# Kernel tuning notes

Measured on AMD Instinct MI355X. Metric: run time of the kernel, lower is better.

The kernel has to match this reference:

```python
import jax, jax.numpy as jnp
import numpy as np

B, S, D = 4, 2048, 1024
H = 16
HD = D // H
FF = 4096
EPS = 1e-5

def _layernorm(x, g, b):
    mu = jnp.mean(x, axis=-1, keepdims=True)
    var = jnp.mean(jnp.square(x - mu), axis=-1, keepdims=True)
    return (x - mu) * jax.lax.rsqrt(var + EPS) * g + b

def setup_inputs() -> dict:
    key = jax.random.key(0)
    ks = jax.random.split(key, 12)
    s_attn = 1.0 / np.sqrt(D)
    s_ff1 = 1.0 / np.sqrt(D)
    s_ff2 = 1.0 / np.sqrt(FF)
    return {
        "x": jax.random.normal(ks[0], (B, S, D), jnp.float32),
        "ln1_g": jnp.ones((D,), jnp.float32),
        "ln1_b": jnp.zeros((D,), jnp.float32),
        "ln2_g": jnp.ones((D,), jnp.float32),
        "ln2_b": jnp.zeros((D,), jnp.float32),
        "Wq": jax.random.normal(ks[1], (D, D), jnp.float32) * s_attn,
        "Wk": jax.random.normal(ks[2], (D, D), jnp.float32) * s_attn,
        "Wv": jax.random.normal(ks[3], (D, D), jnp.float32) * s_attn,
        "Wo": jax.random.normal(ks[4], (D, D), jnp.float32) * s_attn,
        "W1": jax.random.normal(ks[5], (D, FF), jnp.float32) * s_ff1,
        "b1": jnp.zeros((FF,), jnp.float32),
        "W2": jax.random.normal(ks[6], (FF, D), jnp.float32) * s_ff2,
        "b2": jnp.zeros((D,), jnp.float32),
    }

def reference(x, ln1_g, ln1_b, ln2_g, ln2_b, Wq, Wk, Wv, Wo, W1, b1, W2, b2):
    # pre-LN self-attention (y = x), mask=None, dropout=0, attn proj bias=False
    h = _layernorm(x, ln1_g, ln1_b)                      # [B,S,D]
    q = (h @ Wq).reshape(B, S, H, HD).transpose(0, 2, 1, 3)  # [B,H,S,HD]
    k = (h @ Wk).reshape(B, S, H, HD).transpose(0, 2, 1, 3)
    v = (h @ Wv).reshape(B, S, H, HD).transpose(0, 2, 1, 3)
    scores = jnp.einsum('bhqd,bhkd->bhqk', q, k) / np.sqrt(HD)  # [B,H,S,S]
    attn = jax.nn.softmax(scores, axis=-1)
    o = jnp.einsum('bhqk,bhkd->bhqd', attn, v)           # [B,H,S,HD]
    o = o.transpose(0, 2, 1, 3).reshape(B, S, D) @ Wo
    x = x + o
    h2 = _layernorm(x, ln2_g, ln2_b)
    ff = jax.nn.relu(h2 @ W1 + b1) @ W2 + b2             # note: second FC also has relu per FC default
    ff = jax.nn.relu(ff)
    return x + ff
```

## Files before the change

kernel.cpp:

```cpp
#include <hip/hip_runtime.h>
#include <hip/hip_bf16.h>
#include <cstdint>
#include <cstddef>

typedef unsigned short u16;
typedef unsigned int u32;
typedef __bf16 bf16x2 __attribute__((ext_vector_type(2)));
typedef __bf16 bf16x8 __attribute__((ext_vector_type(8)));
typedef float f32x4 __attribute__((ext_vector_type(4)));

#define NB 4
#define NS 2048
#define ND 1024
#define NH 16
#define NHD 64
#define NFF 4096
#define CSC 0.18033688011112042f

#if __has_builtin(__builtin_amdgcn_exp2f)
#define EXP2(x) __builtin_amdgcn_exp2f(x)
#else
#define EXP2(x) exp2f(x)
#endif

__device__ __forceinline__ u16 f2b(float f) {
  union { bf16x2 h; u32 u; } v;
  v.h[0] = (__bf16)f; v.h[1] = (__bf16)f;
  return (u16)(v.u & 0xFFFF);
}
__device__ __forceinline__ u32 pack2(float a, float b) {
  union { bf16x2 h; u32 u; } v;
  v.h[0] = (__bf16)a; v.h[1] = (__bf16)b;
  return v.u;
}

__device__ __forceinline__ void async_copy16(const u16* g, u16* l) {
  __builtin_amdgcn_global_load_lds(
      (const __attribute__((address_space(1))) void*)(const void*)g,
      (__attribute__((address_space(3))) void*)(void*)l, 16, 0, 0);
}

template <int N> __device__ __forceinline__ void vmw() {
  if constexpr (N == 0) asm volatile("s_waitcnt vmcnt(0)" ::: "memory");
  else if constexpr (N == 6) asm volatile("s_waitcnt vmcnt(6)" ::: "memory");
}

__global__ __launch_bounds__(256) void transpose4_f2b(const float* __restrict__ Wq,
                                                      const float* __restrict__ Wk,
                                                      const float* __restrict__ Wv,
                                                      const float* __restrict__ Wo,
                                                      u16* __restrict__ WqkvT,
                                                      u16* __restrict__ WoT) {
  __shared__ float tile[32][33];
  const int z = blockIdx.z;
  const float* in = (z == 0) ? Wq : (z == 1) ? Wk : (z == 2) ? Wv : Wo;
  u16* out = (z < 3) ? WqkvT + (size_t)z * 1024 * 1024 : WoT;
  const int bx = blockIdx.x * 32;
  const int by = blockIdx.y * 32;
  const int tx = threadIdx.x & 31, ty = threadIdx.x >> 5;
#pragma unroll
  for (int i = 0; i < 32; i += 8)
    tile[ty + i][tx] = in[(size_t)(by + ty + i) * 1024 + bx + tx];
  __syncthreads();
#pragma unroll
  for (int i = 0; i < 32; i += 8)
    out[(size_t)(bx + ty + i) * 1024 + by + tx] = f2b(tile[tx][ty + i]);
}

__global__ __launch_bounds__(256) void transpose_f2b(const float* __restrict__ in,
                                                     u16* __restrict__ out,
                                                     int R, int C) {
  __shared__ float tile[32][33];
  const int bx = blockIdx.x * 32;
  const int by = blockIdx.y * 32;
  const int tx = threadIdx.x & 31, ty = threadIdx.x >> 5;
#pragma unroll
  for (int i = 0; i < 32; i += 8)
    tile[ty + i][tx] = in[(size_t)(by + ty + i) * C + bx + tx];
  __syncthreads();
#pragma unroll
  for (int i = 0; i < 32; i += 8)
    out[(size_t)(bx + ty + i) * R + by + tx] = f2b(tile[tx][ty + i]);
}

__global__ __launch_bounds__(256) void ln_kernel(const float* __restrict__ xin,
                                                 const float* __restrict__ g,
                                                 const float* __restrict__ b,
                                                 u16* __restrict__ out) {
  const int row = blockIdx.x;
  const int tid = threadIdx.x;
  const float* p = xin + (size_t)row * ND;
  float v[4];
#pragma unroll
  for (int i = 0; i < 4; i++) v[i] = p[tid + 256 * i];
  float s = 0.f, ss = 0.f;
#pragma unroll
  for (int i = 0; i < 4; i++) { s += v[i]; ss += v[i] * v[i]; }
  for (int off = 32; off > 0; off >>= 1) {
    s += __shfl_down(s, off);
    ss += __shfl_down(ss, off);
  }
  __shared__ float r0[4], r1[4];
  const int w = tid >> 6;
  if ((tid & 63) == 0) { r0[w] = s; r1[w] = ss; }
  __syncthreads();
  s = r0[0] + r0[1] + r0[2] + r0[3];
  ss = r1[0] + r1[1] + r1[2] + r1[3];
  const float mu = s * (1.f / ND);
  const float var = ss * (1.f / ND) - mu * mu;
  const float rstd = rsqrtf(var + 1e-5f);
  u16* o = out + (size_t)row * ND;
#pragma unroll
  for (int i = 0; i < 4; i++) {
    const int c = tid + 256 * i;
    o[c] = f2b((v[i] - mu) * rstd * g[c] + b[c]);
  }
}

template <int OUT_MODE, int RES_MODE, bool BIAS, bool RELU>
__global__ __launch_bounds__(256) void gemm_bt(const u16* __restrict__ A,
                                               const u16* __restrict__ Bt,
                                               const float* __restrict__ bias,
                                               const float* __restrict__ res,
                                               void* __restrict__ out,
                                               u16* __restrict__ outK,
                                               u16* __restrict__ outV,
                                               int M, int N, int K) {
  __shared__ __align__(16) u16 lA[2][128 * 64];
  __shared__ __align__(16) u16 lB[2][128 * 64];
  const int tid = threadIdx.x;
  const int bm = blockIdx.y * 128, bn = blockIdx.x * 128;
  const int w = tid >> 6, lane = tid & 63, quad = lane >> 4, l16 = lane & 15;
  const int wm = (w & 1) * 64, wn = (w >> 1) * 64;
  const int sw = l16 & 7;

  f32x4 acc[4][4];
#pragma unroll
  for (int i = 0; i < 4; i++)
#pragma unroll
    for (int j = 0; j < 4; j++) acc[i][j] = (f32x4){0.f, 0.f, 0.f, 0.f};

  const int srow = w * 8 + (lane >> 3);
  const int sch = (lane & 7) ^ ((lane >> 3) & 7);
  const u16* Ap = A + (size_t)(bm + srow) * K + sch * 8;
  const u16* Bp = Bt + (size_t)(bn + srow) * K + sch * 8;
  const int NT = K >> 6;

#pragma unroll
  for (int c = 0; c < 4; c++)
    async_copy16(Ap + (size_t)c * 32 * K, &lA[0][(c * 32 + w * 8) * 64]);
#pragma unroll
  for (int c = 0; c < 4; c++)
    async_copy16(Bp + (size_t)c * 32 * K, &lB[0][(c * 32 + w * 8) * 64]);

  for (int kt = 0; kt < NT; ++kt) {
    const int cur = kt & 1;
    __syncthreads();
    if (kt + 1 < NT) {
      const size_t koff = (size_t)(kt + 1) * 64;
#pragma unroll
      for (int c = 0; c < 4; c++)
        async_copy16(Ap + (size_t)c * 32 * K + koff,
                     &lA[cur ^ 1][(c * 32 + w * 8) * 64]);
#pragma unroll
      for (int c = 0; c < 4; c++)
        async_copy16(Bp + (size_t)c * 32 * K + koff,
                     &lB[cur ^ 1][(c * 32 + w * 8) * 64]);
    }
    const u16* lAc = lA[cur];
    const u16* lBc = lB[cur];
#pragma unroll
    for (int x = 0; x < 2; x++) {
      bf16x8 af[4], bf[4];
#pragma unroll
      for (int i = 0; i < 4; i++)
        af[i] = *(const bf16x8*)&lAc[(wm + i * 16 + l16) * 64 + ((x * 4 + quad) ^ sw) * 8];
#pragma unroll
      for (int j = 0; j < 4; j++)
        bf[j] = *(const bf16x8*)&lBc[(wn + j * 16 + l16) * 64 + ((x * 4 + quad) ^ sw) * 8];
#pragma unroll
      for (int i = 0; i < 4; i++)
#pragma unroll
        for (int j = 0; j < 4; j++)
          acc[i][j] = __builtin_amdgcn_mfma_f32_16x16x32_bf16(af[i], bf[j], acc[i][j], 0, 0, 0);
    }
  }

  if constexpr (OUT_MODE == 3) {
    const int m0 = bm + wm;
#pragma unroll
    for (int i = 0; i < 4; i++) {
#pragma unroll
      for (int j = 0; j < 4; j++) {
        const int n = bn + wn + j * 16 + l16;
        const int mB = m0 + i * 16 + quad * 4;
        const int bb = mB >> 11, s = mB & 2047;
        if (bn < 1024) {
          const int hh = n >> 6, hd = n & 63;
          u16* o = (u16*)out + (((size_t)(bb * NH + hh) * NS + s) * NHD + hd);
#pragma unroll
          for (int r = 0; r < 4; r++) o[(size_t)r * NHD] = f2b(acc[i][j][r] * CSC);
        } else if (bn < 2048) {
          const int nk = n - 1024;
          const int hh = nk >> 6, hd = nk & 63;
          u16* o = outK + (((size_t)(bb * NH + hh) * NS + s) * NHD + hd);
#pragma unroll
          for (int r = 0; r < 4; r++) o[(size_t)r * NHD] = f2b(acc[i][j][r]);
        } else {
          const int nv = n - 2048;
          const int hh = nv >> 6, hd = nv & 63;
          uint2 pk = make_uint2(pack2(acc[i][j][0], acc[i][j][1]),
                                pack2(acc[i][j][2], acc[i][j][3]));
          *(uint2*)&outV[((size_t)(bb * NH + hh) * NHD + hd) * NS + s] = pk;
        }
      }
    }
  } else {
#pragma unroll
    for (int i = 0; i < 4; i++) {
#pragma unroll
      for (int r = 0; r < 4; r++) {
        const int m = bm + wm + i * 16 + quad * 4 + r;
#pragma unroll
        for (int j = 0; j < 4; j++) {
          const int n = bn + wn + j * 16 + l16;
          float vv = acc[i][j][r];
          if constexpr (BIAS) vv += bias[n];
          if constexpr (RELU) vv = fmaxf(vv, 0.f);
          if constexpr (RES_MODE == 1) vv += res[(size_t)m * N + n];
          if constexpr (OUT_MODE == 0) {
            ((u16*)out)[(size_t)m * N + n] = f2b(vv);
          } else {
            ((float*)out)[(size_t)m * N + n] = vv;
          }
        }
      }
    }
  }
}

template <bool BIAS, bool RELU>
__global__ __launch_bounds__(512, 2) void gemm_8ph(const u16* __restrict__ A,
                                                   const u16* __restrict__ Bt,
                                                   const float* __restrict__ bias,
                                                   u16* __restrict__ out,
                                                   int M, int N, int K) {
  __shared__ __align__(16) u16 lA[2][256 * 64];
  __shared__ __align__(16) u16 lB[2][256 * 64];
  const int tid = threadIdx.x;
  const int w = tid >> 6, lane = tid & 63, quad = lane >> 4, l16 = lane & 15;
  const int sw = l16 & 7;
  const int wr = w >> 2, wc = w & 3;

  const int nb = gridDim.x, chunk = nb >> 3;
  const int wg = ((int)blockIdx.x & 7) * chunk + ((int)blockIdx.x >> 3);
  const int nby = M >> 8;
  const int bx = wg / nby, by = wg % nby;
  const int bm = by * 256, bn = bx * 256;

  f32x4 acc[8][4];
#pragma unroll
  for (int i = 0; i < 8; i++)
#pragma unroll
    for (int j = 0; j < 4; j++) acc[i][j] = (f32x4){0.f, 0.f, 0.f, 0.f};

  const int srow = w * 8 + (lane >> 3);
  const int sch = (lane & 7) ^ ((lane >> 3) & 7);
  const u16* Ap = A + (size_t)(bm + srow) * K + sch * 8;
  const u16* Bp = Bt + (size_t)(bn + srow) * K + sch * 8;
  const int NT = K >> 6;

  auto stA = [&](int t, int h) {
    async_copy16(Ap + (size_t)(h * 64) * K + (size_t)t * 64,
                 &lA[t & 1][(h * 64 + w * 8) * 64]);
  };
  auto stB = [&](int t, int h) {
    async_copy16(Bp + (size_t)(h * 64) * K + (size_t)t * 64,
                 &lB[t & 1][(h * 64 + w * 8) * 64]);
  };

  stA(0, 0); stA(0, 1); stA(0, 2); stA(0, 3);
  stB(0, 0); stB(0, 1); stB(0, 2); stB(0, 3);
  stB(1, 0); stB(1, 1); stB(1, 2); stB(1, 3);
  stA(1, 0); stA(1, 2);
  vmw<6>();
  __builtin_amdgcn_s_barrier();
  __builtin_amdgcn_sched_barrier(0);

  for (int kt = 0; kt < NT; ++kt) {
    const u16* lAc = lA[kt & 1];
    const u16* lBc = lB[kt & 1];
    bf16x8 bfr[4][2];
#pragma unroll
    for (int p = 0; p < 4; ++p) {
      bf16x8 af[2][2];
#pragma unroll
      for (int ii = 0; ii < 2; ii++)
#pragma unroll
        for (int x = 0; x < 2; x++)
          af[ii][x] = *(const bf16x8*)&lAc[(wr * 128 + (p * 2 + ii) * 16 + l16) * 64 +
                                           ((x * 4 + quad) ^ sw) * 8];
      if (p == 0) {
#pragma unroll
        for (int j = 0; j < 4; j++)
#pragma unroll
          for (int x = 0; x < 2; x++)
            bfr[j][x] = *(const bf16x8*)&lBc[(wc * 64 + j * 16 + l16) * 64 +
                                             ((x * 4 + quad) ^ sw) * 8];
        if (kt + 1 < NT) { stA(kt + 1, 1); stA(kt + 1, 3); }
      } else if (p == 1) {
        if (kt + 2 < NT) { stB(kt + 2, 0); stB(kt + 2, 1); }
      } else if (p == 2) {
        if (kt + 2 < NT) { stB(kt + 2, 2); stB(kt + 2, 3); }
      } else {
        if (kt + 2 < NT) { stA(kt + 2, 0); stA(kt + 2, 2); }
      }
      __builtin_amdgcn_s_barrier();
      __builtin_amdgcn_sched_barrier(0);
      __builtin_amdgcn_s_setprio(1);
#pragma unroll
      for (int ii = 0; ii < 2; ii++)
#pragma unroll
        for (int j = 0; j < 4; j++)
#pragma unroll
          for (int x = 0; x < 2; x++)
            acc[p * 2 + ii][j] = __builtin_amdgcn_mfma_f32_16x16x32_bf16(
                af[ii][x], bfr[j][x], acc[p * 2 + ii][j], 0, 0, 0);
      __builtin_amdgcn_s_setprio(0);
      if (p == 3) {
        if (kt + 2 < NT) {
          vmw<6>();
          __builtin_amdgcn_sched_barrier(0);
        } else if (kt + 1 < NT) {
          vmw<0>();
          __builtin_amdgcn_sched_barrier(0);
        }
      }
      __builtin_amdgcn_s_barrier();
      __builtin_amdgcn_sched_barrier(0);
    }
  }

#pragma unroll
  for (int i = 0; i < 8; i++) {
#pragma unroll
    for (int r = 0; r < 4; r++) {
      const int m = bm + wr * 128 + i * 16 + quad * 4 + r;
#pragma unroll
      for (int j = 0; j < 4; j++) {
        const int n = bn + wc * 64 + j * 16 + l16;
        float vv = acc[i][j][r];
        if constexpr (BIAS) vv += bias[n];
        if constexpr (RELU) vv = fmaxf(vv, 0.f);
        out[(size_t)m * N + n] = f2b(vv);
      }
    }
  }
}

#define OSTR 72
__global__ __launch_bounds__(256, 4) void attn_kernel(const u16* __restrict__ Q,
                                                      const u16* __restrict__ K,
                                                      const u16* __restrict__ VT,
                                                      u16* __restrict__ O) {
  __shared__ __align__(16) u16 lK[128 * 64];
  __shared__ __align__(16) u16 lV[64 * 128];
  const int tid = threadIdx.x;
  const int w = tid >> 6, lane = tid & 63, quad = lane >> 4, l16 = lane & 15;
  const int sw = l16 & 7;

  const int bid = blockIdx.x;
  const int xcd = bid & 7, slot = bid >> 3;
  const int bh = xcd + 8 * (slot >> 5);
  const int q0 = (slot & 31) * 64;
  const size_t base = (size_t)bh * NS * NHD;

  const u16* qrow = Q + base + (size_t)(q0 + w * 16 + l16) * NHD;
  bf16x8 qf[2];
  qf[0] = *(const bf16x8*)(qrow + quad * 8);
  qf[1] = *(const bf16x8*)(qrow + 32 + quad * 8);

  const int krow = w * 8 + (lane >> 3);
  const int kch = (lane & 7) ^ ((lane >> 3) & 7);
  const int vrow = w * 4 + (lane >> 4);
  const int vch = (lane & 15) ^ (vrow & 7);
  const u16* kp = K + base + (size_t)krow * 64 + kch * 8;
  const u16* vp = VT + base + (size_t)vrow * NS + vch * 8;

  float l_i = 0.f;
  f32x4 oa[4];
#pragma unroll
  for (int jo = 0; jo < 4; jo++) oa[jo] = (f32x4){0.f, 0.f, 0.f, 0.f};

  for (int kt = 0; kt < NS / 128; ++kt) {
    __syncthreads();
#pragma unroll
    for (int c = 0; c < 4; c++)
      async_copy16(kp + (size_t)c * 32 * 64, &lK[(c * 32 + w * 8) * 64]);
#pragma unroll
    for (int c = 0; c < 4; c++)
      async_copy16(vp + (size_t)c * 16 * NS, &lV[(c * 16 + w * 4) * 128]);
    __syncthreads();
    kp += 128 * 64;
    vp += 128;

    f32x4 sc[8];
#pragma unroll
    for (int j = 0; j < 8; j++) sc[j] = (f32x4){0.f, 0.f, 0.f, 0.f};
    __builtin_amdgcn_s_setprio(1);
#pragma unroll
    for (int x = 0; x < 2; x++)
#pragma unroll
      for (int j = 0; j < 8; j++) {
        bf16x8 kf = *(const bf16x8*)&lK[(j * 16 + l16) * 64 + ((x * 4 + quad) ^ sw) * 8];
        sc[j] = __builtin_amdgcn_mfma_f32_16x16x32_bf16(kf, qf[x], sc[j], 0, 0, 0);
      }
    __builtin_amdgcn_s_setprio(0);

    float rsum = 0.f;
#pragma unroll
    for (int j = 0; j < 8; j++) {
#pragma unroll
      for (int r = 0; r < 4; r++) sc[j][r] = EXP2(sc[j][r]);
      rsum += (sc[j][0] + sc[j][1]) + (sc[j][2] + sc[j][3]);
    }
    rsum += __shfl_xor(rsum, 16);
    rsum += __shfl_xor(rsum, 32);
    l_i += rsum;

#pragma unroll
    for (int x = 0; x < 4; x++) {
      u32 A0 = pack2(sc[2 * x][0], sc[2 * x][1]);
      u32 A1 = pack2(sc[2 * x][2], sc[2 * x][3]);
      u32 B0 = pack2(sc[2 * x + 1][0], sc[2 * x + 1][1]);
      u32 B1 = pack2(sc[2 * x + 1][2], sc[2 * x + 1][3]);
      asm("v_permlane32_swap_b32 %0, %1" : "+v"(A0), "+v"(B0));
      asm("v_permlane32_swap_b32 %0, %1" : "+v"(A1), "+v"(B1));
      asm("v_permlane16_swap_b32 %0, %1" : "+v"(A0), "+v"(B0));
      asm("v_permlane16_swap_b32 %0, %1" : "+v"(A1), "+v"(B1));
      union { u32 u[4]; bf16x8 h; } bq;
      bq.u[0] = A0; bq.u[1] = A1; bq.u[2] = B0; bq.u[3] = B1;
      __builtin_amdgcn_s_setprio(1);
#pragma unroll
      for (int jo = 0; jo < 4; jo++) {
        bf16x8 av = *(const bf16x8*)&lV[(jo * 16 + l16) * 128 + ((x * 4 + quad) ^ sw) * 8];
        oa[jo] = __builtin_amdgcn_mfma_f32_16x16x32_bf16(av, bq.h, oa[jo], 0, 0, 0);
      }
      __builtin_amdgcn_s_setprio(0);
    }
  }

  __syncthreads();
  const float inv = 1.f / l_i;
  u16* lo = &lK[w * 16 * OSTR];
#pragma unroll
  for (int jo = 0; jo < 4; jo++)
#pragma unroll
    for (int pr = 0; pr < 2; pr++)
      *(u32*)&lo[l16 * OSTR + jo * 16 + quad * 4 + pr * 2] =
          pack2(oa[jo][2 * pr] * inv, oa[jo][2 * pr + 1] * inv);

  const int bb = bh >> 4, hh = bh & 15;
#pragma unroll
  for (int t = 0; t < 2; t++) {
    const int row = t * 8 + (lane >> 3);
    const int seg = lane & 7;
    bf16x8 ov = *(const bf16x8*)&lo[row * OSTR + seg * 8];
    const int srow = q0 + w * 16 + row;
    *(int4*)&O[((size_t)bb * NS + srow) * ND + hh * 64 + seg * 8] = *(int4*)&ov;
  }
}

extern "C" void kernel_launch(void* const* d_in, const int* in_sizes, int n_in,
                              void* d_out, int out_size, void* d_ws, size_t ws_size,
                              hipStream_t stream) {
  (void)in_sizes; (void)n_in; (void)out_size; (void)ws_size;
  const float* x = (const float*)d_in[0];
  const float* ln1g = (const float*)d_in[1];
  const float* ln1b = (const float*)d_in[2];
  const float* ln2g = (const float*)d_in[3];
  const float* ln2b = (const float*)d_in[4];
  const float* Wq = (const float*)d_in[5];
  const float* Wk = (const float*)d_in[6];
  const float* Wv = (const float*)d_in[7];
  const float* Wo = (const float*)d_in[8];
  const float* W1 = (const float*)d_in[9];
  const float* b1 = (const float*)d_in[10];
  const float* W2 = (const float*)d_in[11];
  const float* b2 = (const float*)d_in[12];

  u16* ws = (u16*)d_ws;
  u16* h     = ws;
  u16* WqkvT = ws + (size_t)8  * 1048576;
  u16* WoT   = ws + (size_t)11 * 1048576;
  u16* W1T   = ws + (size_t)12 * 1048576;
  u16* W2T   = ws + (size_t)16 * 1048576;
  u16* qb    = ws + (size_t)20 * 1048576;
  u16* kb    = ws + (size_t)28 * 1048576;
  u16* vt    = ws + (size_t)36 * 1048576;
  u16* ob    = ws + (size_t)44 * 1048576;
  float* x2  = (float*)(ws + (size_t)52 * 1048576);
  u16* ff    = qb;
  u16* h2    = h;

  const int M = NB * NS;

  transpose4_f2b<<<dim3(32, 32, 4), 256, 0, stream>>>(Wq, Wk, Wv, Wo, WqkvT, WoT);
  transpose_f2b<<<dim3(128, 32), 256, 0, stream>>>(W1, W1T, ND, NFF);
  transpose_f2b<<<dim3(32, 128), 256, 0, stream>>>(W2, W2T, NFF, ND);

  ln_kernel<<<M, 256, 0, stream>>>(x, ln1g, ln1b, h);

  gemm_bt<3, 0, false, false><<<dim3(24, 64), 256, 0, stream>>>(
      h, WqkvT, nullptr, nullptr, qb, kb, vt, M, 3072, ND);

  attn_kernel<<<dim3(2048), 256, 0, stream>>>(qb, kb, vt, ob);

  gemm_bt<2, 1, false, false><<<dim3(8, 64), 256, 0, stream>>>(
      ob, WoT, nullptr, x, x2, nullptr, nullptr, M, ND, ND);

  ln_kernel<<<M, 256, 0, stream>>>(x2, ln2g, ln2b, h2);

  gemm_8ph<true, true><<<512, 512, 0, stream>>>(h2, W1T, b1, ff, M, NFF, ND);

  gemm_bt<2, 1, true, true><<<dim3(8, 64), 256, 0, stream>>>(
      ff, W2T, b2, x2, d_out, nullptr, nullptr, M, ND, NFF);
}
```

Baseline: 493.9 us.

## Vectorize layernorm, single-buffer GEMM LDS, and widen attention blocks to 128 queries

```diff
diff --git a/kernel.cpp b/kernel.cpp
--- a/kernel.cpp
+++ b/kernel.cpp
@@ -89,13 +89,9 @@
                                                  u16* __restrict__ out) {
   const int row = blockIdx.x;
   const int tid = threadIdx.x;
-  const float* p = xin + (size_t)row * ND;
-  float v[4];
-#pragma unroll
-  for (int i = 0; i < 4; i++) v[i] = p[tid + 256 * i];
-  float s = 0.f, ss = 0.f;
-#pragma unroll
-  for (int i = 0; i < 4; i++) { s += v[i]; ss += v[i] * v[i]; }
+  const float4 v = *(const float4*)(xin + (size_t)row * ND + tid * 4);
+  float s = (v.x + v.y) + (v.z + v.w);
+  float ss = (v.x * v.x + v.y * v.y) + (v.z * v.z + v.w * v.w);
   for (int off = 32; off > 0; off >>= 1) {
     s += __shfl_down(s, off);
     ss += __shfl_down(ss, off);
@@ -109,12 +105,13 @@
   const float mu = s * (1.f / ND);
   const float var = ss * (1.f / ND) - mu * mu;
   const float rstd = rsqrtf(var + 1e-5f);
-  u16* o = out + (size_t)row * ND;
-#pragma unroll
-  for (int i = 0; i < 4; i++) {
-    const int c = tid + 256 * i;
-    o[c] = f2b((v[i] - mu) * rstd * g[c] + b[c]);
-  }
+  const float4 gv = *(const float4*)(g + tid * 4);
+  const float4 bv = *(const float4*)(b + tid * 4);
+  uint2 pk = make_uint2(pack2((v.x - mu) * rstd * gv.x + bv.x,
+                              (v.y - mu) * rstd * gv.y + bv.y),
+                        pack2((v.z - mu) * rstd * gv.z + bv.z,
+                              (v.w - mu) * rstd * gv.w + bv.w));
+  *(uint2*)(out + (size_t)row * ND + tid * 4) = pk;
 }
 
 template <int OUT_MODE, int RES_MODE, bool BIAS, bool RELU>
@@ -126,8 +123,8 @@
                                                u16* __restrict__ outK,
                                                u16* __restrict__ outV,
                                                int M, int N, int K) {
-  __shared__ __align__(16) u16 lA[2][128 * 64];
-  __shared__ __align__(16) u16 lB[2][128 * 64];
+  __shared__ __align__(16) u16 lA[128 * 64];
+  __shared__ __align__(16) u16 lB[128 * 64];
   const int tid = threadIdx.x;
   const int bm = blockIdx.y * 128, bn = blockIdx.x * 128;
   const int w = tid >> 6, lane = tid & 63, quad = lane >> 4, l16 = lane & 15;
@@ -144,40 +141,25 @@
   const int sch = (lane & 7) ^ ((lane >> 3) & 7);
   const u16* Ap = A + (size_t)(bm + srow) * K + sch * 8;
   const u16* Bp = Bt + (size_t)(bn + srow) * K + sch * 8;
-  const int NT = K >> 6;
-
-#pragma unroll
-  for (int c = 0; c < 4; c++)
-    async_copy16(Ap + (size_t)c * 32 * K, &lA[0][(c * 32 + w * 8) * 64]);
-#pragma unroll
-  for (int c = 0; c < 4; c++)
-    async_copy16(Bp + (size_t)c * 32 * K, &lB[0][(c * 32 + w * 8) * 64]);
-
-  for (int kt = 0; kt < NT; ++kt) {
-    const int cur = kt & 1;
+
+  for (int k0 = 0; k0 < K; k0 += 64) {
     __syncthreads();
-    if (kt + 1 < NT) {
-      const size_t koff = (size_t)(kt + 1) * 64;
-#pragma unroll
-      for (int c = 0; c < 4; c++)
-        async_copy16(Ap + (size_t)c * 32 * K + koff,
-                     &lA[cur ^ 1][(c * 32 + w * 8) * 64]);
-#pragma unroll
-      for (int c = 0; c < 4; c++)
-        async_copy16(Bp + (size_t)c * 32 * K + koff,
-                     &lB[cur ^ 1][(c * 32 + w * 8) * 64]);
-    }
-    const u16* lAc = lA[cur];
-    const u16* lBc = lB[cur];
+#pragma unroll
+    for (int c = 0; c < 4; c++)
+      async_copy16(Ap + (size_t)c * 32 * K + k0, &lA[(c * 32 + w * 8) * 64]);
+#pragma unroll
+    for (int c = 0; c < 4; c++)
+      async_copy16(Bp + (size_t)c * 32 * K + k0, &lB[(c * 32 + w * 8) * 64]);
+    __syncthreads();
 #pragma unroll
     for (int x = 0; x < 2; x++) {
       bf16x8 af[4], bf[4];
 #pragma unroll
       for (int i = 0; i < 4; i++)
-        af[i] = *(const bf16x8*)&lAc[(wm + i * 16 + l16) * 64 + ((x * 4 + quad) ^ sw) * 8];
+        af[i] = *(const bf16x8*)&lA[(wm + i * 16 + l16) * 64 + ((x * 4 + quad) ^ sw) * 8];
 #pragma unroll
       for (int j = 0; j < 4; j++)
-        bf[j] = *(const bf16x8*)&lBc[(wn + j * 16 + l16) * 64 + ((x * 4 + quad) ^ sw) * 8];
+        bf[j] = *(const bf16x8*)&lB[(wn + j * 16 + l16) * 64 + ((x * 4 + quad) ^ sw) * 8];
 #pragma unroll
       for (int i = 0; i < 4; i++)
 #pragma unroll
@@ -359,20 +341,21 @@
 }
 
 #define OSTR 72
-__global__ __launch_bounds__(256, 4) void attn_kernel(const u16* __restrict__ Q,
+__global__ __launch_bounds__(512, 8) void attn_kernel(const u16* __restrict__ Q,
                                                       const u16* __restrict__ K,
                                                       const u16* __restrict__ VT,
                                                       u16* __restrict__ O) {
-  __shared__ __align__(16) u16 lK[128 * 64];
-  __shared__ __align__(16) u16 lV[64 * 128];
+  __shared__ __align__(16) u16 lds[128 * 64 + 64 * 128];
+  u16* lK = lds;
+  u16* lV = lds + 128 * 64;
   const int tid = threadIdx.x;
   const int w = tid >> 6, lane = tid & 63, quad = lane >> 4, l16 = lane & 15;
   const int sw = l16 & 7;
 
   const int bid = blockIdx.x;
   const int xcd = bid & 7, slot = bid >> 3;
-  const int bh = xcd + 8 * (slot >> 5);
-  const int q0 = (slot & 31) * 64;
+  const int bh = xcd + 8 * (slot >> 4);
+  const int q0 = (slot & 15) * 128;
   const size_t base = (size_t)bh * NS * NHD;
 
   const u16* qrow = Q + base + (size_t)(q0 + w * 16 + l16) * NHD;
@@ -380,12 +363,12 @@
   qf[0] = *(const bf16x8*)(qrow + quad * 8);
   qf[1] = *(const bf16x8*)(qrow + 32 + quad * 8);
 
-  const int krow = w * 8 + (lane >> 3);
+  const int krow = w * 16 + (lane >> 3);
   const int kch = (lane & 7) ^ ((lane >> 3) & 7);
-  const int vrow = w * 4 + (lane >> 4);
-  const int vch = (lane & 15) ^ (vrow & 7);
   const u16* kp = K + base + (size_t)krow * 64 + kch * 8;
-  const u16* vp = VT + base + (size_t)vrow * NS + vch * 8;
+  const int vr0 = w * 8 + (lane >> 4), vr1 = vr0 + 4;
+  const u16* vp0 = VT + base + (size_t)vr0 * NS + ((lane & 15) ^ (vr0 & 7)) * 8;
+  const u16* vp1 = VT + base + (size_t)vr1 * NS + ((lane & 15) ^ (vr1 & 7)) * 8;
 
   float l_i = 0.f;
   f32x4 oa[4];
@@ -394,15 +377,14 @@
 
   for (int kt = 0; kt < NS / 128; ++kt) {
     __syncthreads();
-#pragma unroll
-    for (int c = 0; c < 4; c++)
-      async_copy16(kp + (size_t)c * 32 * 64, &lK[(c * 32 + w * 8) * 64]);
-#pragma unroll
-    for (int c = 0; c < 4; c++)
-      async_copy16(vp + (size_t)c * 16 * NS, &lV[(c * 16 + w * 4) * 128]);
+    async_copy16(kp, &lK[(w * 16) * 64]);
+    async_copy16(kp + 8 * 64, &lK[(w * 16 + 8) * 64]);
+    async_copy16(vp0, &lV[(w * 8) * 128]);
+    async_copy16(vp1, &lV[(w * 8 + 4) * 128]);
     __syncthreads();
     kp += 128 * 64;
-    vp += 128;
+    vp0 += 128;
+    vp1 += 128;
 
     f32x4 sc[8];
 #pragma unroll
@@ -452,7 +434,7 @@
 
   __syncthreads();
   const float inv = 1.f / l_i;
-  u16* lo = &lK[w * 16 * OSTR];
+  u16* lo = &lds[w * 16 * OSTR];
 #pragma unroll
   for (int jo = 0; jo < 4; jo++)
 #pragma unroll
@@ -514,7 +496,7 @@
   gemm_bt<3, 0, false, false><<<dim3(24, 64), 256, 0, stream>>>(
       h, WqkvT, nullptr, nullptr, qb, kb, vt, M, 3072, ND);
 
-  attn_kernel<<<dim3(2048), 256, 0, stream>>>(qb, kb, vt, ob);
+  attn_kernel<<<dim3(1024), 512, 0, stream>>>(qb, kb, vt, ob);
 
   gemm_bt<2, 1, false, false><<<dim3(8, 64), 256, 0, stream>>>(
       ob, WoT, nullptr, x, x2, nullptr, nullptr, M, ND, ND);
```

After: 590.4 us. 19.5% more time.
